# Kernel optimization log

Hardware: AMD Instinct MI355X
Metric: run time of the kernel (lower is better)

The kernel has to match this reference:

```python
import jax, jax.numpy as jnp
import numpy as np

EPS = 1e-06


def setup_inputs() -> dict:
    key = jax.random.key(0)
    k1, k2 = jax.random.split(key)
    N, C, H, W = 256, 3, 256, 256
    preds = jax.random.normal(k1, (N, C, H, W), dtype=jnp.float32)
    targets = jax.random.normal(k2, (N, C, H, W), dtype=jnp.float32)
    return {"preds": preds, "targets": targets}


def reference(preds, targets):
    N = preds.shape[0]
    # Flatten to [N, D] as in torch's .view(len, -1)
    Z = targets.reshape(N, -1)  # targets first, matching the torch call order
    B = preds.reshape(N, -1)
    Z_c = Z - jnp.mean(Z, axis=1, keepdims=True)
    B_c = B - jnp.mean(B, axis=1, keepdims=True)
    # Full N x N cross-correlation matrix (faithful to original), then diagonal
    num = jnp.einsum('nd,md->nm', Z_c, B_c)
    Z_norm = jnp.linalg.norm(Z_c, axis=1, keepdims=True)  # [N,1]
    B_norm = jnp.linalg.norm(B_c, axis=1, keepdims=True)  # [N,1]
    denom = Z_norm @ B_norm.T  # [N,N]
    pearson = num / (denom + EPS)
    corr = jnp.diagonal(pearson)  # [N]
    return jnp.mean(corr)  # reduction='mean'
```

## Files before the change

### kernel.cpp

```cpp
#include <hip/hip_runtime.h>
#include <stdint.h>


typedef float f4 __attribute__((ext_vector_type(4)));

constexpr int    NROWS    = 256;
constexpr int    D        = 3 * 256 * 256;
constexpr int    D4       = D / 4;
constexpr int    TPB      = 256;
constexpr int    WPB      = TPB / 64;
constexpr int    WPR      = 8;
constexpr int    NBLOCKS  = NROWS * WPR / WPB;
constexpr int    K        = 4;
constexpr int    STAGE_F4 = 64 * K;
constexpr int    WAVE_F4  = D4 / WPR;
constexpr int    NSTAGES  = WAVE_F4 / STAGE_F4;
constexpr double EPS      = 1e-6;

__device__ __forceinline__ void async_ld16(const void* g, void* l) {
    __builtin_amdgcn_global_load_lds(
        (const __attribute__((address_space(1))) uint32_t*)g,
        (__attribute__((address_space(3))) uint32_t*)l,
        16, 0, 2);
}

__global__ __launch_bounds__(TPB, 2) void partial_kernel(
        const f4* __restrict__ preds,
        const f4* __restrict__ targets,
        double* __restrict__ partials)
{
    __shared__ f4 sBuf[WPB][2][2][K][64];

    const int  tid  = threadIdx.x;
    const int  w    = tid >> 6;
    const int  lane = tid & 63;
    const int  gw   = blockIdx.x * WPB + w;
    const int  row  = gw >> 3;
    const int  seg  = gw & (WPR - 1);
    const long gbase = (long)row * D4 + (long)seg * WAVE_F4;

    auto issue = [&](int t, int p) {
        const long gb = gbase + (long)t * STAGE_F4;
        #pragma unroll
        for (int u = 0; u < K; ++u) {
            async_ld16(&preds[gb + u * 64 + lane],   &sBuf[w][p][0][u][0]);
            async_ld16(&targets[gb + u * 64 + lane], &sBuf[w][p][1][u][0]);
        }
    };

    issue(0, 0);
    issue(1, 1);

    double sZ = 0, sB = 0, sZZ = 0, sBB = 0, sZB = 0;

    auto accum = [&](const f4* bv, const f4* zv) {
        #pragma unroll
        for (int u = 0; u < K; ++u) {
            #pragma unroll
            for (int c = 0; c < 4; ++c) {
                const double b = (double)bv[u][c];
                const double z = (double)zv[u][c];
                sZ += z; sB += b;
                sZZ = fma(z, z, sZZ);
                sBB = fma(b, b, sBB);
                sZB = fma(z, b, sZB);
            }
        }
    };

    for (int t = 0; t < NSTAGES - 1; ++t) {
        const int p = t & 1;
        asm volatile("s_waitcnt vmcnt(8)" ::: "memory");
        __builtin_amdgcn_sched_barrier(0);
        f4 bv[K], zv[K];
        #pragma unroll
        for (int u = 0; u < K; ++u) {
            bv[u] = sBuf[w][p][0][u][lane];
            zv[u] = sBuf[w][p][1][u][lane];
        }
        asm volatile("s_waitcnt lgkmcnt(0)" ::: "memory");
        __builtin_amdgcn_sched_barrier(0);
        if (t + 2 < NSTAGES) issue(t + 2, p);
        accum(bv, zv);
    }
    {
        const int p = (NSTAGES - 1) & 1;
        asm volatile("s_waitcnt vmcnt(0)" ::: "memory");
        __builtin_amdgcn_sched_barrier(0);
        f4 bv[K], zv[K];
        #pragma unroll
        for (int u = 0; u < K; ++u) {
            bv[u] = sBuf[w][p][0][u][lane];
            zv[u] = sBuf[w][p][1][u][lane];
        }
        asm volatile("s_waitcnt lgkmcnt(0)" ::: "memory");
        accum(bv, zv);
    }

    #pragma unroll
    for (int off = 32; off > 0; off >>= 1) {
        sZ  += __shfl_down(sZ,  off);
        sB  += __shfl_down(sB,  off);
        sZZ += __shfl_down(sZZ, off);
        sBB += __shfl_down(sBB, off);
        sZB += __shfl_down(sZB, off);
    }
    if (lane == 0) {
        double* o = partials + (long)gw * 5;
        o[0] = sZ; o[1] = sB; o[2] = sZZ; o[3] = sBB; o[4] = sZB;
    }
}

__global__ __launch_bounds__(NROWS) void finalize_kernel(
        const double* __restrict__ partials, float* __restrict__ out)
{
    const int r = threadIdx.x;
    const double* p = partials + (long)r * WPR * 5;
    double tZ = 0, tB = 0, tZZ = 0, tBB = 0, tZB = 0;
    #pragma unroll
    for (int s = 0; s < WPR; ++s) {
        tB  += p[s * 5 + 1 - 1 + 0];
    }
    tZ = 0; tB = 0; tZZ = 0; tBB = 0; tZB = 0;
    #pragma unroll
    for (int s = 0; s < WPR; ++s) {
        tZ  += p[s * 5 + 0];
        tB  += p[s * 5 + 1];
        tZZ += p[s * 5 + 2];
        tBB += p[s * 5 + 3];
        tZB += p[s * 5 + 4];
    }
    const double invD = 1.0 / (double)D;
    const double num  = tZB - tZ * tB * invD;
    const double varZ = fmax(tZZ - tZ * tZ * invD, 0.0);
    const double varB = fmax(tBB - tB * tB * invD, 0.0);
    const double den  = sqrt(varZ) * sqrt(varB) + EPS;
    double corr = num / den;

    #pragma unroll
    for (int off = 32; off > 0; off >>= 1) corr += __shfl_down(corr, off);

    __shared__ double sm[NROWS / 64];
    const int wave = r >> 6;
    const int lane = r & 63;
    if (lane == 0) sm[wave] = corr;
    __syncthreads();
    if (r == 0) {
        double t = 0.0;
        #pragma unroll
        for (int v = 0; v < NROWS / 64; ++v) t += sm[v];
        out[0] = (float)(t / (double)NROWS);
    }
}

extern "C" void kernel_launch(void* const* d_in, const int* in_sizes, int n_in,
                              void* d_out, int out_size, void* d_ws, size_t ws_size,
                              hipStream_t stream) {
    const f4* preds   = (const f4*)d_in[0];
    const f4* targets = (const f4*)d_in[1];
    double* partials  = (double*)d_ws;
    float*  out       = (float*)d_out;

    hipLaunchKernelGGL(partial_kernel, dim3(NBLOCKS), dim3(TPB), 0, stream,
                       preds, targets, partials);
    hipLaunchKernelGGL(finalize_kernel, dim3(1), dim3(NROWS), 0, stream,
                       partials, out);
}
```

Baseline: 357.3 us.

## Replace async LDS staging with register double-buffered nontemporal loads per block

The per-wave global_load_lds pipeline through shared memory is replaced by direct nontemporal vector loads into registers with a two-deep software prefetch. Each row is now split across 8 blocks of 256 threads, with a block-level shared-memory reduction before the partials are written. This removes the LDS round trip and the manual waitcnt scheduling, so the loop is simpler. In exchange, fewer loads are in flight per wave, which the compiler's scheduling has to make up for, and the block now pays a __syncthreads.

```diff
diff --git a/kernel.cpp b/kernel.cpp
--- a/kernel.cpp
+++ b/kernel.cpp
@@ -4,98 +4,59 @@
 
 typedef float f4 __attribute__((ext_vector_type(4)));
 
-constexpr int    NROWS    = 256;
-constexpr int    D        = 3 * 256 * 256;
-constexpr int    D4       = D / 4;
-constexpr int    TPB      = 256;
-constexpr int    WPB      = TPB / 64;
-constexpr int    WPR      = 8;
-constexpr int    NBLOCKS  = NROWS * WPR / WPB;
-constexpr int    K        = 4;
-constexpr int    STAGE_F4 = 64 * K;
-constexpr int    WAVE_F4  = D4 / WPR;
-constexpr int    NSTAGES  = WAVE_F4 / STAGE_F4;
-constexpr double EPS      = 1e-6;
+constexpr int    NROWS   = 256;
+constexpr int    D       = 3 * 256 * 256;
+constexpr int    D4      = D / 4;
+constexpr int    BPR     = 8;
+constexpr int    NBLOCKS = NROWS * BPR;
+constexpr int    TPB     = 256;
+constexpr int    SPAN    = D4 / BPR;
+constexpr int    ITER    = SPAN / TPB;
+constexpr double EPS     = 1e-6;
 
-__device__ __forceinline__ void async_ld16(const void* g, void* l) {
-    __builtin_amdgcn_global_load_lds(
-        (const __attribute__((address_space(1))) uint32_t*)g,
-        (__attribute__((address_space(3))) uint32_t*)l,
-        16, 0, 2);
-}
-
-__global__ __launch_bounds__(TPB, 2) void partial_kernel(
+__global__ __launch_bounds__(TPB) void partial_kernel(
         const f4* __restrict__ preds,
         const f4* __restrict__ targets,
         double* __restrict__ partials)
 {
-    __shared__ f4 sBuf[WPB][2][2][K][64];
+    const int  tid  = threadIdx.x;
+    const int  blk  = blockIdx.x;
+    const int  row  = blk >> 3;
+    const int  oct  = blk & (BPR - 1);
+    const long base = (long)row * D4 + (long)oct * SPAN + tid;
 
-    const int  tid  = threadIdx.x;
-    const int  w    = tid >> 6;
-    const int  lane = tid & 63;
-    const int  gw   = blockIdx.x * WPB + w;
-    const int  row  = gw >> 3;
-    const int  seg  = gw & (WPR - 1);
-    const long gbase = (long)row * D4 + (long)seg * WAVE_F4;
+    double sZ = 0, sB = 0, sZZ = 0, sBB = 0, sZB = 0;
 
-    auto issue = [&](int t, int p) {
-        const long gb = gbase + (long)t * STAGE_F4;
+    auto accum = [&](const f4 bv, const f4 zv) {
         #pragma unroll
-        for (int u = 0; u < K; ++u) {
-            async_ld16(&preds[gb + u * 64 + lane],   &sBuf[w][p][0][u][0]);
-            async_ld16(&targets[gb + u * 64 + lane], &sBuf[w][p][1][u][0]);
+        for (int c = 0; c < 4; ++c) {
+            const double b = (double)bv[c];
+            const double z = (double)zv[c];
+            sZ += z; sB += b;
+            sZZ = fma(z, z, sZZ);
+            sBB = fma(b, b, sBB);
+            sZB = fma(z, b, sZB);
         }
     };
 
-    issue(0, 0);
-    issue(1, 1);
+    f4 pc0 = __builtin_nontemporal_load(&preds[base]);
+    f4 pc1 = __builtin_nontemporal_load(&preds[base + TPB]);
+    f4 tc0 = __builtin_nontemporal_load(&targets[base]);
+    f4 tc1 = __builtin_nontemporal_load(&targets[base + TPB]);
 
-    double sZ = 0, sB = 0, sZZ = 0, sBB = 0, sZB = 0;
-
-    auto accum = [&](const f4* bv, const f4* zv) {
-        #pragma unroll
-        for (int u = 0; u < K; ++u) {
-            #pragma unroll
-            for (int c = 0; c < 4; ++c) {
-                const double b = (double)bv[u][c];
-                const double z = (double)zv[u][c];
-                sZ += z; sB += b;
-                sZZ = fma(z, z, sZZ);
-                sBB = fma(b, b, sBB);
-                sZB = fma(z, b, sZB);
-            }
-        }
-    };
-
-    for (int t = 0; t < NSTAGES - 1; ++t) {
-        const int p = t & 1;
-        asm volatile("s_waitcnt vmcnt(8)" ::: "memory");
-        __builtin_amdgcn_sched_barrier(0);
-        f4 bv[K], zv[K];
-        #pragma unroll
-        for (int u = 0; u < K; ++u) {
-            bv[u] = sBuf[w][p][0][u][lane];
-            zv[u] = sBuf[w][p][1][u][lane];
-        }
-        asm volatile("s_waitcnt lgkmcnt(0)" ::: "memory");
-        __builtin_amdgcn_sched_barrier(0);
-        if (t + 2 < NSTAGES) issue(t + 2, p);
-        accum(bv, zv);
+    #pragma unroll 1
+    for (int i = 0; i < ITER - 2; i += 2) {
+        const long nb = base + (long)(i + 2) * TPB;
+        const f4 pn0 = __builtin_nontemporal_load(&preds[nb]);
+        const f4 pn1 = __builtin_nontemporal_load(&preds[nb + TPB]);
+        const f4 tn0 = __builtin_nontemporal_load(&targets[nb]);
+        const f4 tn1 = __builtin_nontemporal_load(&targets[nb + TPB]);
+        accum(pc0, tc0);
+        accum(pc1, tc1);
+        pc0 = pn0; pc1 = pn1; tc0 = tn0; tc1 = tn1;
     }
-    {
-        const int p = (NSTAGES - 1) & 1;
-        asm volatile("s_waitcnt vmcnt(0)" ::: "memory");
-        __builtin_amdgcn_sched_barrier(0);
-        f4 bv[K], zv[K];
-        #pragma unroll
-        for (int u = 0; u < K; ++u) {
-            bv[u] = sBuf[w][p][0][u][lane];
-            zv[u] = sBuf[w][p][1][u][lane];
-        }
-        asm volatile("s_waitcnt lgkmcnt(0)" ::: "memory");
-        accum(bv, zv);
-    }
+    accum(pc0, tc0);
+    accum(pc1, tc1);
 
     #pragma unroll
     for (int off = 32; off > 0; off >>= 1) {
@@ -105,9 +66,22 @@
         sBB += __shfl_down(sBB, off);
         sZB += __shfl_down(sZB, off);
     }
+
+    constexpr int NWAVES = TPB / 64;
+    __shared__ double sm[5][NWAVES];
+    const int w    = tid >> 6;
+    const int lane = tid & 63;
     if (lane == 0) {
-        double* o = partials + (long)gw * 5;
-        o[0] = sZ; o[1] = sB; o[2] = sZZ; o[3] = sBB; o[4] = sZB;
+        sm[0][w] = sZ;  sm[1][w] = sB;
+        sm[2][w] = sZZ; sm[3][w] = sBB;
+        sm[4][w] = sZB;
+    }
+    __syncthreads();
+    if (tid == 0) {
+        double* o = partials + (long)blk * 5;
+        #pragma unroll
+        for (int k = 0; k < 5; ++k)
+            o[k] = sm[k][0] + sm[k][1] + sm[k][2] + sm[k][3];
     }
 }
 
@@ -115,15 +89,10 @@
         const double* __restrict__ partials, float* __restrict__ out)
 {
     const int r = threadIdx.x;
-    const double* p = partials + (long)r * WPR * 5;
+    const double* p = partials + (long)r * BPR * 5;
     double tZ = 0, tB = 0, tZZ = 0, tBB = 0, tZB = 0;
     #pragma unroll
-    for (int s = 0; s < WPR; ++s) {
-        tB  += p[s * 5 + 1 - 1 + 0];
-    }
-    tZ = 0; tB = 0; tZZ = 0; tBB = 0; tZB = 0;
-    #pragma unroll
-    for (int s = 0; s < WPR; ++s) {
+    for (int s = 0; s < BPR; ++s) {
         tZ  += p[s * 5 + 0];
         tB  += p[s * 5 + 1];
         tZZ += p[s * 5 + 2];
```

Measured after the change: 357.6 us. No clear change (+0.1%).
